# Performance work log

Measured on AMD Instinct MI355X. Metric: run time of the kernel, lower is better.

## Reference

```python
import jax, jax.numpy as jnp
import numpy as np

B, T, D, E, V, EXTRA = 32, 1024, 512, 256, 50257, 200


def setup_inputs() -> dict:
    key = jax.random.key(0)
    ks = jax.random.split(key, 20)
    s = 0.02
    rn = lambda k, shape: jax.random.normal(k, shape, dtype=jnp.float32) * s
    inp = {}
    inp["decoder_input"] = jax.random.randint(ks[0], (B,), 0, V)
    inp["h0"] = rn(ks[1], (B, D))
    inp["c0"] = rn(ks[2], (B, D))
    inp["encoder_outputs"] = rn(ks[3], (B, T, 2 * D))
    inp["encoder_pad_mask"] = jnp.ones((B, T), jnp.float32)
    inp["previous_context_vector"] = rn(ks[4], (B, 2 * D))
    inp["coverage"] = jax.random.uniform(ks[5], (B, T), jnp.float32) * 0.01
    inp["extra_zeros"] = jnp.zeros((B, EXTRA), jnp.float32)
    inp["encoder_input_extra_vocabs"] = jax.random.randint(ks[6], (B, T), 0, V + EXTRA)
    inp["step"] = 1
    inp["embedding"] = rn(ks[7], (V, E))
    inp["W_gx"] = rn(ks[8], (2 * D + E, E)); inp["b_gx"] = jnp.zeros((E,), jnp.float32)
    inp["W_ih"] = rn(ks[9], (E, 4 * D)); inp["W_hh"] = rn(ks[10], (D, 4 * D))
    inp["b_ih"] = jnp.zeros((4 * D,), jnp.float32); inp["b_hh"] = jnp.zeros((4 * D,), jnp.float32)
    inp["W_h"] = rn(ks[11], (2 * D, 2 * D))
    inp["W_c"] = rn(ks[12], (2 * D,))
    inp["W_s"] = rn(ks[13], (2 * D, 2 * D)); inp["b_s"] = jnp.zeros((2 * D,), jnp.float32)
    inp["v"] = rn(ks[14], (2 * D,))
    inp["W_pg"] = rn(ks[15], (4 * D + E,)); inp["b_pg"] = jnp.zeros((1,), jnp.float32)
    inp["W_v1"] = rn(ks[16], (3 * D, D)); inp["b_v1"] = jnp.zeros((D,), jnp.float32)
    inp["W_v2"] = rn(ks[17], (D, V)); inp["b_v2"] = jnp.zeros((V,), jnp.float32)
    return inp


def reference(decoder_input, h0, c0, encoder_outputs, encoder_pad_mask,
              previous_context_vector, coverage, extra_zeros,
              encoder_input_extra_vocabs, step,
              embedding, W_gx, b_gx, W_ih, W_hh, b_ih, b_hh,
              W_h, W_c, W_s, b_s, v, W_pg, b_pg, W_v1, b_v1, W_v2, b_v2):
    # Pointer-generator decoder single step (training path / step>0), coverage on.
    softmax_temperature = 1.0
    emb = embedding[decoder_input]                                  # [B,E]
    x = jnp.concatenate([previous_context_vector, emb], -1) @ W_gx + b_gx  # [B,E]
    # LSTM cell, torch gate order (i, f, g, o)
    gates = x @ W_ih + h0 @ W_hh + b_ih + b_hh                      # [B,4D]
    i, f, g, o = jnp.split(gates, 4, axis=-1)
    c1 = jax.nn.sigmoid(f) * c0 + jax.nn.sigmoid(i) * jnp.tanh(g)
    h1 = jax.nn.sigmoid(o) * jnp.tanh(c1)                           # [B,D]
    dec_hat = jnp.concatenate([h1, c1], -1)                         # [B,2D]
    # Bahdanau additive attention with coverage feature
    enc_feat = encoder_outputs @ W_h                                # [B,T,2D]
    dec_feat = dec_hat @ W_s + b_s                                  # [B,2D]
    cov_feat = coverage[..., None] * W_c                            # [B,T,2D]
    energy = jnp.tanh(enc_feat + dec_feat[:, None, :] + cov_feat)
    scores = energy @ v                                             # [B,T]
    att = jax.nn.softmax(scores / softmax_temperature, axis=-1) * encoder_pad_mask
    att = att / att.sum(-1, keepdims=True)                          # renormalized
    context = jnp.einsum('bt,btd->bd', att, encoder_outputs)        # [B,2D]
    coverage_next = coverage + att
    # pointer-generator gate
    pg_in = jnp.concatenate([context, dec_hat, x], -1)              # [B,4D+E]
    p_gen = jax.nn.sigmoid(pg_in @ W_pg + b_pg)[:, None]            # [B,1]
    out = jnp.concatenate([h1, context], -1)                        # [B,3D]
    logits = ((out @ W_v1 + b_v1) @ W_v2 + b_v2) / softmax_temperature
    vocab_dist = jax.nn.softmax(logits, axis=-1)                    # [B,V]
    vd_oov = jnp.concatenate([p_gen * vocab_dist, extra_zeros], 1)  # [B,V+EXTRA]
    att_oov = (1.0 - p_gen) * att                                   # [B,T]
    rows = jnp.arange(B)[:, None]
    vocab_dist_final = vd_oov.at[rows, encoder_input_extra_vocabs].add(att_oov)
    return (vocab_dist_final, (h1, c1), context, att, coverage_next)
```

## Files before the change

kernel.cpp:

```cpp
#include <hip/hip_runtime.h>
#include <hip/hip_bf16.h>

typedef __attribute__((ext_vector_type(4))) float f32x4;
typedef __attribute__((ext_vector_type(8))) short s16x8;
typedef __attribute__((ext_vector_type(4))) short s16x4;

#define DEVINL __device__ __forceinline__

static constexpr int BB = 32, TT = 1024, DD = 512, EE = 256, VV = 50257, EXTRA = 200;
static constexpr int D2 = 1024;
static constexpr int VE = VV + EXTRA;
static constexpr long MM = (long)BB * TT;
static constexpr int VPAD = 50304;

DEVINL unsigned short f2bf(float x) {
    union { float f; unsigned int u; } c; c.f = x;
    unsigned int u = c.u;
    u += 0x7fffu + ((u >> 16) & 1u);
    return (unsigned short)(u >> 16);
}
DEVINL float bf2f(unsigned short h) {
    union { unsigned int u; float f; } c; c.u = ((unsigned int)h) << 16;
    return c.f;
}
DEVINL float sigmoidf_(float x) { return 1.0f / (1.0f + __expf(-x)); }
DEVINL float tanh_fast(float x) {
    x = fminf(15.f, fmaxf(-15.f, x));
    float e = __expf(2.f * x);
    return (e - 1.f) / (e + 1.f);
}
DEVINL void gl16(const void* g, void* l) {
    __builtin_amdgcn_global_load_lds((__attribute__((address_space(1))) void*)g,
                                     (__attribute__((address_space(3))) void*)l, 16, 0, 0);
}

__global__ void k_transpose_wh(const float* __restrict__ Wh, unsigned short* __restrict__ WhT) {
    __shared__ float tile[32][33];
    int n0 = blockIdx.x * 32, k0 = blockIdx.y * 32;
    int tx = threadIdx.x, ty = threadIdx.y;
    #pragma unroll
    for (int i = 0; i < 4; i++)
        tile[ty + i * 8][tx] = Wh[(long)(k0 + ty + i * 8) * D2 + n0 + tx];
    __syncthreads();
    #pragma unroll
    for (int i = 0; i < 4; i++) {
        int n = n0 + ty + i * 8;
        int kcol = (k0 + tx) ^ ((n & 7) << 3);
        WhT[(long)n * D2 + kcol] = f2bf(tile[tx][ty + i * 8]);
    }
}

__global__ void k_enc2bf(const float* __restrict__ enc, unsigned short* __restrict__ dst) {
    long idx = (long)blockIdx.x * 256 + threadIdx.x;
    int m  = (int)(idx >> 7);
    int k2 = (int)(idx & 127) * 8;
    int s  = (m & 7) << 3;
    const float* src = enc + (long)m * 1024 + (k2 ^ s);
    f32x4 a = *(const f32x4*)src;
    f32x4 b = *(const f32x4*)(src + 4);
    s16x8 h;
    h[0] = (short)f2bf(a[0]); h[1] = (short)f2bf(a[1]); h[2] = (short)f2bf(a[2]); h[3] = (short)f2bf(a[3]);
    h[4] = (short)f2bf(b[0]); h[5] = (short)f2bf(b[1]); h[6] = (short)f2bf(b[2]); h[7] = (short)f2bf(b[3]);
    *(s16x8*)(dst + (long)m * 1024 + k2) = h;
}

__global__ void k_wv2t(const float* __restrict__ Wv2, unsigned short* __restrict__ out) {
    __shared__ float tile[32][33];
    int v0 = blockIdx.x * 32, k0 = blockIdx.y * 32;
    int tx = threadIdx.x, ty = threadIdx.y;
    #pragma unroll
    for (int i = 0; i < 4; i++) {
        int k = k0 + ty + i * 8;
        int v = v0 + tx;
        tile[ty + i * 8][tx] = (v < VV) ? Wv2[(long)k * VV + v] : 0.f;
    }
    __syncthreads();
    #pragma unroll
    for (int i = 0; i < 4; i++) {
        int v = v0 + ty + i * 8;
        int kcol = (k0 + tx) ^ ((v & 7) << 3);
        out[(long)v * 512 + kcol] = f2bf(tile[tx][ty + i * 8]);
    }
}

__global__ __launch_bounds__(512) void k_x(
    const int* __restrict__ dec_in, const float* __restrict__ pcv,
    const float* __restrict__ embt, const float* __restrict__ Wgx,
    const float* __restrict__ bgx, float* __restrict__ xbuf) {
    __shared__ float xs[1280];
    __shared__ float sred[8][64];
    int b = blockIdx.x, n0 = blockIdx.y * 64;
    int tid = threadIdx.x, nl = tid & 63, ks = tid >> 6;
    long er = (long)dec_in[b] * EE;
    for (int i = tid; i < 1280; i += 512)
        xs[i] = (i < 1024) ? pcv[b * 1024 + i] : embt[er + i - 1024];
    __syncthreads();
    float acc = 0.f;
    for (int k = ks * 160; k < ks * 160 + 160; ++k)
        acc += xs[k] * Wgx[(long)k * EE + n0 + nl];
    sred[ks][nl] = acc;
    __syncthreads();
    if (tid < 64) {
        int n = n0 + tid;
        float s = bgx[n];
        #pragma unroll
        for (int i = 0; i < 8; i++) s += sred[i][tid];
        xbuf[b * EE + n] = s;
    }
}

__global__ __launch_bounds__(512) void k_lstm(
    const float* __restrict__ xbuf, const float* __restrict__ h0,
    const float* __restrict__ c0, const float* __restrict__ Wih,
    const float* __restrict__ Whh, const float* __restrict__ bih,
    const float* __restrict__ bhh, float* __restrict__ h1o,
    float* __restrict__ c1o, float* __restrict__ dechat) {
    __shared__ float xs[768];
    __shared__ float sred[4][8][64];
    int b = blockIdx.x, d0 = blockIdx.y * 64;
    int tid = threadIdx.x, dl = tid & 63, ks = tid >> 6;
    for (int i = tid; i < 768; i += 512)
        xs[i] = (i < 256) ? xbuf[b * 256 + i] : h0[b * 512 + i - 256];
    __syncthreads();
    float a0 = 0, a1 = 0, a2 = 0, a3 = 0;
    for (int k = ks * 96; k < ks * 96 + 96; ++k) {
        float xv = xs[k];
        const float* wr = (k < 256) ? (Wih + (long)k * 2048) : (Whh + (long)(k - 256) * 2048);
        a0 += xv * wr[d0 + dl];        a1 += xv * wr[512 + d0 + dl];
        a2 += xv * wr[1024 + d0 + dl]; a3 += xv * wr[1536 + d0 + dl];
    }
    sred[0][ks][dl] = a0; sred[1][ks][dl] = a1; sred[2][ks][dl] = a2; sred[3][ks][dl] = a3;
    __syncthreads();
    if (tid < 64) {
        int d = d0 + tid;
        float gi = bih[d] + bhh[d];
        float gf = bih[512 + d] + bhh[512 + d];
        float gg = bih[1024 + d] + bhh[1024 + d];
        float go = bih[1536 + d] + bhh[1536 + d];
        #pragma unroll
        for (int s = 0; s < 8; s++) {
            gi += sred[0][s][tid]; gf += sred[1][s][tid];
            gg += sred[2][s][tid]; go += sred[3][s][tid];
        }
        float c1 = sigmoidf_(gf) * c0[b * 512 + d] + sigmoidf_(gi) * tanh_fast(gg);
        float h1 = sigmoidf_(go) * tanh_fast(c1);
        h1o[b * 512 + d] = h1; c1o[b * 512 + d] = c1;
        dechat[b * 1024 + d] = h1; dechat[b * 1024 + 512 + d] = c1;
    }
}

__global__ __launch_bounds__(512) void k_decfeat(
    const float* __restrict__ dechat, const float* __restrict__ Ws,
    const float* __restrict__ bs, float* __restrict__ decfeat) {
    __shared__ float xs[1024];
    __shared__ float sred[8][64];
    int b = blockIdx.x, n0 = blockIdx.y * 64;
    int tid = threadIdx.x, nl = tid & 63, ks = tid >> 6;
    for (int i = tid; i < 1024; i += 512) xs[i] = dechat[b * 1024 + i];
    __syncthreads();
    float acc = 0.f;
    for (int k = ks * 128; k < ks * 128 + 128; ++k)
        acc += xs[k] * Ws[(long)k * 1024 + n0 + nl];
    sred[ks][nl] = acc;
    __syncthreads();
    if (tid < 64) {
        int n = n0 + tid;
        float s = bs[n];
        #pragma unroll
        for (int i = 0; i < 8; i++) s += sred[i][tid];
        decfeat[b * 1024 + n] = s;
    }
}

__global__ __launch_bounds__(512) void k_scores(
    const unsigned short* __restrict__ encswz, const unsigned short* __restrict__ whtswz,
    const float* __restrict__ decfeat, const float* __restrict__ cov,
    const float* __restrict__ Wc, const float* __restrict__ vvec,
    float* __restrict__ scorep) {
    __shared__ __align__(16) unsigned short As[128 * 64];
    __shared__ __align__(16) unsigned short Bs[256 * 64];
    __shared__ float sred[4][128];
    const int tid = threadIdx.x;
    const int lane = tid & 63, wave = tid >> 6;
    const int wid = __builtin_amdgcn_readfirstlane(wave);
    const int g = lane >> 4, c = lane & 15;
    const int wm = wave >> 2, wn = wave & 3;

    const int bid = blockIdx.x;
    const int xcd = bid & 7, t = bid >> 3;
    const int mt = xcd * 32 + (t >> 2), nt = t & 3;
    const long m0 = (long)mt * 128;
    const int n0 = nt * 256;
    const int bblk = mt >> 3;

    const int arow = wid * 16 + (lane >> 3);
    const int axo  = (lane & 7) * 8;
    const int brow = wid * 32 + (lane >> 3);
    unsigned short* aBase = &As[wid * 1024];
    unsigned short* bBase = &Bs[wid * 2048];

    f32x4 acc[4][4];
    #pragma unroll
    for (int i = 0; i < 4; i++)
        #pragma unroll
        for (int j = 0; j < 4; j++) acc[i][j] = (f32x4){0.f, 0.f, 0.f, 0.f};

    const int sx = (c & 7) << 3;

    for (int kt = 0; kt < 16; ++kt) {
        const int k0 = kt * 64;
        __syncthreads();
        gl16(encswz + (m0 + arow) * 1024 + k0 + axo,       aBase);
        gl16(encswz + (m0 + arow + 8) * 1024 + k0 + axo,   aBase + 512);
        gl16(whtswz + (long)(n0 + brow) * 1024 + k0 + axo,        bBase);
        gl16(whtswz + (long)(n0 + brow + 8) * 1024 + k0 + axo,    bBase + 512);
        gl16(whtswz + (long)(n0 + brow + 16) * 1024 + k0 + axo,   bBase + 1024);
        gl16(whtswz + (long)(n0 + brow + 24) * 1024 + k0 + axo,   bBase + 1536);
        __syncthreads();
        #pragma unroll
        for (int kk = 0; kk < 2; ++kk) {
            const int kse = (kk * 32 + g * 8) ^ sx;
            s16x8 af[4], bfj[4];
            #pragma unroll
            for (int i = 0; i < 4; i++) af[i] = *(const s16x8*)&As[(wm * 64 + i * 16 + c) * 64 + kse];
            #pragma unroll
            for (int j = 0; j < 4; j++) bfj[j] = *(const s16x8*)&Bs[(wn * 64 + j * 16 + c) * 64 + kse];
            #pragma unroll
            for (int i = 0; i < 4; i++)
                #pragma unroll
                for (int j = 0; j < 4; j++)
                    acc[i][j] = __builtin_amdgcn_mfma_f32_16x16x32_bf16(af[i], bfj[j], acc[i][j], 0, 0, 0);
        }
    }
    float dfv[4], wcv[4], vvj[4];
    #pragma unroll
    for (int j = 0; j < 4; j++) {
        int col = n0 + wn * 64 + j * 16 + c;
        dfv[j] = decfeat[bblk * D2 + col];
        wcv[j] = Wc[col];
        vvj[j] = vvec[col];
    }
    float sAcc[4][4];
    #pragma unroll
    for (int i = 0; i < 4; i++) {
        #pragma unroll
        for (int r = 0; r < 4; r++) {
            const long m = m0 + wm * 64 + i * 16 + g * 4 + r;
            const float covm = cov[m];
            float su = 0.f;
            #pragma unroll
            for (int j = 0; j < 4; j++) {
                float e = acc[i][j][r] + dfv[j] + covm * wcv[j];
                su += tanh_fast(e) * vvj[j];
            }
            su += __shfl_xor(su, 1); su += __shfl_xor(su, 2);
            su += __shfl_xor(su, 4); su += __shfl_xor(su, 8);
            sAcc[i][r] = su;
        }
    }
    if (c == 0) {
        #pragma unroll
        for (int i = 0; i < 4; i++)
            #pragma unroll
            for (int r = 0; r < 4; r++)
                sred[wn][wm * 64 + i * 16 + g * 4 + r] = sAcc[i][r];
    }
    __syncthreads();
    if (tid < 128)
        scorep[(long)nt * MM + m0 + tid] = sred[0][tid] + sred[1][tid] + sred[2][tid] + sred[3][tid];
}

__global__ void k_softmax(const float* __restrict__ scorep, const float* __restrict__ mask,
                          const float* __restrict__ cov, float* __restrict__ att,
                          float* __restrict__ covn) {
    int b = blockIdx.x, tid = threadIdx.x;
    __shared__ float sm[8];
    float sv[4];
    float mx = -1e30f;
    #pragma unroll
    for (int i = 0; i < 4; i++) {
        long idx = (long)b * TT + tid + 256 * i;
        sv[i] = scorep[idx] + scorep[MM + idx] + scorep[2 * MM + idx] + scorep[3 * MM + idx];
        mx = fmaxf(mx, sv[i]);
    }
    for (int o = 32; o; o >>= 1) mx = fmaxf(mx, __shfl_xor(mx, o));
    if ((tid & 63) == 0) sm[tid >> 6] = mx;
    __syncthreads();
    mx = fmaxf(fmaxf(sm[0], sm[1]), fmaxf(sm[2], sm[3]));
    __syncthreads();
    float e[4]; float s = 0.f;
    #pragma unroll
    for (int i = 0; i < 4; i++) { e[i] = __expf(sv[i] - mx); s += e[i]; }
    for (int o = 32; o; o >>= 1) s += __shfl_xor(s, o);
    if ((tid & 63) == 0) sm[tid >> 6] = s;
    __syncthreads();
    s = sm[0] + sm[1] + sm[2] + sm[3];
    __syncthreads();
    float inv = 1.f / s;
    float am[4]; float s2 = 0.f;
    #pragma unroll
    for (int i = 0; i < 4; i++) { am[i] = e[i] * inv * mask[b * TT + tid + 256 * i]; s2 += am[i]; }
    for (int o = 32; o; o >>= 1) s2 += __shfl_xor(s2, o);
    if ((tid & 63) == 0) sm[tid >> 6] = s2;
    __syncthreads();
    s2 = sm[0] + sm[1] + sm[2] + sm[3];
    float inv2 = 1.f / s2;
    #pragma unroll
    for (int i = 0; i < 4; i++) {
        int t = tid + 256 * i;
        float a = am[i] * inv2;
        att[b * TT + t] = a;
        covn[b * TT + t] = cov[b * TT + t] + a;
    }
}

__global__ void k_context(const unsigned short* __restrict__ encswz, const float* __restrict__ att,
                          float* __restrict__ part) {
    int b = blockIdx.x, tc = blockIdx.y;
    int d4 = threadIdx.x;
    float a0 = 0, a1 = 0, a2 = 0, a3 = 0;
    const float* ab = att + b * TT;
    for (int t = tc * 64; t < tc * 64 + 64; ++t) {
        float a = ab[t];
        int sx = (t & 7) << 3;
        const unsigned short* ep = encswz + ((long)b * TT + t) * D2 + ((d4 * 4) ^ sx);
        s16x4 ev = *(const s16x4*)ep;
        a0 += a * bf2f((unsigned short)ev[0]); a1 += a * bf2f((unsigned short)ev[1]);
        a2 += a * bf2f((unsigned short)ev[2]); a3 += a * bf2f((unsigned short)ev[3]);
    }
    float* pp = part + (long)tc * BB * D2 + b * D2 + d4 * 4;
    pp[0] = a0; pp[1] = a1; pp[2] = a2; pp[3] = a3;
}

__global__ void k_ctxreduce(const float* __restrict__ part, float* __restrict__ ctx) {
    int i = blockIdx.x * 256 + threadIdx.x;
    float s = 0.f;
    #pragma unroll
    for (int p = 0; p < 16; p++) s += part[(long)p * BB * D2 + i];
    ctx[i] = s;
}

__global__ void k_pgen(const float* __restrict__ ctx, const float* __restrict__ dechat,
                       const float* __restrict__ xbuf, const float* __restrict__ Wpg,
                       const float* __restrict__ bpg, float* __restrict__ pgen) {
    int b = blockIdx.x, tid = threadIdx.x;
    __shared__ float sm[8];
    float acc = 0.f;
    for (int k = tid; k < D2; k += 256)
        acc += ctx[b * D2 + k] * Wpg[k] + dechat[b * D2 + k] * Wpg[D2 + k];
    acc += xbuf[b * EE + tid] * Wpg[2 * D2 + tid];
    for (int o = 32; o; o >>= 1) acc += __shfl_xor(acc, o);
    if ((tid & 63) == 0) sm[tid >> 6] = acc;
    __syncthreads();
    if (tid == 0) {
        float t = sm[0] + sm[1] + sm[2] + sm[3];
        pgen[b] = sigmoidf_(t + bpg[0]);
    }
}

__global__ __launch_bounds__(512) void k_hidden(
    const float* __restrict__ h1, const float* __restrict__ ctx,
    const float* __restrict__ Wv1, const float* __restrict__ bv1,
    unsigned short* __restrict__ hbf) {
    __shared__ float xs[1536];
    __shared__ float sred[8][64];
    int b = blockIdx.x, n0 = blockIdx.y * 64;
    int tid = threadIdx.x, nl = tid & 63, ks = tid >> 6;
    for (int i = tid; i < 1536; i += 512)
        xs[i] = (i < 512) ? h1[b * 512 + i] : ctx[b * 1024 + i - 512];
    __syncthreads();
    float acc = 0.f;
    for (int k = ks * 192; k < ks * 192 + 192; ++k)
        acc += xs[k] * Wv1[(long)k * 512 + n0 + nl];
    sred[ks][nl] = acc;
    __syncthreads();
    if (tid < 64) {
        int n = n0 + tid;
        float s = bv1[n];
        #pragma unroll
        for (int i = 0; i < 8; i++) s += sred[i][tid];
        hbf[b * 512 + n] = f2bf(s);
    }
}

__global__ __launch_bounds__(256) void k_logits(const unsigned short* __restrict__ hbf,
                                                const unsigned short* __restrict__ wv2t,
                                                const float* __restrict__ bv2,
                                                float* __restrict__ logits) {
    __shared__ __align__(16) unsigned short Bs[64 * 128];
    const int tid = threadIdx.x;
    const int lane = tid & 63, wave = tid >> 6;
    const int wid = __builtin_amdgcn_readfirstlane(wave);
    const int g = lane >> 4, c = lane & 15;
    const int wm = wave >> 1, wn = wave & 1;
    const long v0 = (long)blockIdx.x * 64;

    const int srow = wid * 16 + (lane >> 4);
    const int scol = (lane & 15) * 8;
    unsigned short* bBase = &Bs[wid * 16 * 128];

    f32x4 acc[2];
    acc[0] = (f32x4){0.f, 0.f, 0.f, 0.f};
    acc[1] = (f32x4){0.f, 0.f, 0.f, 0.f};
    const int sx = (c & 7) << 3;

    for (int kt = 0; kt < 4; ++kt) {
        const int k0 = kt * 128;
        __syncthreads();
        #pragma unroll
        for (int i = 0; i < 4; i++)
            gl16(wv2t + (v0 + srow + i * 4) * 512 + k0 + scol, bBase + i * 512);
        __syncthreads();
        #pragma unroll
        for (int kk = 0; kk < 4; ++kk) {
            const int kse = (kk * 32 + g * 8) ^ sx;
            s16x8 af = *(const s16x8*)&hbf[(wm * 16 + c) * 512 + k0 + (kk * 32 + g * 8)];
            s16x8 bf0 = *(const s16x8*)&Bs[(wn * 32 + c) * 128 + kse];
            s16x8 bf1 = *(const s16x8*)&Bs[(wn * 32 + 16 + c) * 128 + kse];
            acc[0] = __builtin_amdgcn_mfma_f32_16x16x32_bf16(af, bf0, acc[0], 0, 0, 0);
            acc[1] = __builtin_amdgcn_mfma_f32_16x16x32_bf16(af, bf1, acc[1], 0, 0, 0);
        }
    }
    #pragma unroll
    for (int j = 0; j < 2; j++) {
        long v = v0 + wn * 32 + j * 16 + c;
        if (v < VV) {
            float bvv = bv2[v];
            #pragma unroll
            for (int r = 0; r < 4; r++) {
                int b = wm * 16 + g * 4 + r;
                logits[(long)b * VV + v] = acc[j][r] + bvv;
            }
        }
    }
}

__global__ __launch_bounds__(1024) void k_vocab_all(
    const float* __restrict__ logits, const float* __restrict__ pgen,
    const float* __restrict__ extraz, const float* __restrict__ att,
    const int* __restrict__ eiv, float* __restrict__ out0) {
    int b = blockIdx.x, tid = threadIdx.x;
    __shared__ float sm[16];
    const float* lr = logits + (long)b * VV;
    float mx = -1e30f;
    for (int v = tid; v < VV; v += 1024) mx = fmaxf(mx, lr[v]);
    for (int o = 32; o; o >>= 1) mx = fmaxf(mx, __shfl_xor(mx, o));
    if ((tid & 63) == 0) sm[tid >> 6] = mx;
    __syncthreads();
    #pragma unroll
    for (int i = 0; i < 16; i++) mx = fmaxf(mx, sm[i]);
    __syncthreads();
    float s = 0.f;
    for (int v = tid; v < VV; v += 1024) s += __expf(lr[v] - mx);
    for (int o = 32; o; o >>= 1) s += __shfl_xor(s, o);
    if ((tid & 63) == 0) sm[tid >> 6] = s;
    __syncthreads();
    s = 0.f;
    #pragma unroll
    for (int i = 0; i < 16; i++) s += sm[i];
    float pg = pgen[b];
    float inv = pg / s;
    float* orow = out0 + (long)b * VE;
    for (int v = tid; v < VV; v += 1024) orow[v] = __expf(lr[v] - mx) * inv;
    if (tid < EXTRA) orow[VV + tid] = extraz[b * EXTRA + tid];
    __syncthreads();
    float a = (1.f - pg) * att[b * TT + tid];
    atomicAdd(orow + eiv[b * TT + tid], a);
}

extern "C" void kernel_launch(void* const* d_in, const int* in_sizes, int n_in,
                              void* d_out, int out_size, void* d_ws, size_t ws_size,
                              hipStream_t stream) {
    const int*   dec_in = (const int*)d_in[0];
    const float* h0     = (const float*)d_in[1];
    const float* c0     = (const float*)d_in[2];
    const float* enc    = (const float*)d_in[3];
    const float* mask   = (const float*)d_in[4];
    const float* pcv    = (const float*)d_in[5];
    const float* cov    = (const float*)d_in[6];
    const float* extraz = (const float*)d_in[7];
    const int*   eiv    = (const int*)d_in[8];
    const float* embt   = (const float*)d_in[10];
    const float* Wgx    = (const float*)d_in[11];
    const float* bgx    = (const float*)d_in[12];
    const float* Wih    = (const float*)d_in[13];
    const float* Whh    = (const float*)d_in[14];
    const float* bih    = (const float*)d_in[15];
    const float* bhh    = (const float*)d_in[16];
    const float* Wh     = (const float*)d_in[17];
    const float* Wc     = (const float*)d_in[18];
    const float* Ws     = (const float*)d_in[19];
    const float* bs     = (const float*)d_in[20];
    const float* vv     = (const float*)d_in[21];
    const float* Wpg    = (const float*)d_in[22];
    const float* bpg    = (const float*)d_in[23];
    const float* Wv1    = (const float*)d_in[24];
    const float* bv1    = (const float*)d_in[25];
    const float* Wv2    = (const float*)d_in[26];
    const float* bv2    = (const float*)d_in[27];

    float* out = (float*)d_out;
    float* out_vd  = out;
    float* out_h1  = out + (long)BB * VE;
    float* out_c1  = out_h1 + BB * DD;
    float* out_ctx = out_c1 + BB * DD;
    float* out_att = out_ctx + BB * D2;
    float* out_cov = out_att + BB * TT;

    char* p = (char*)d_ws;
    unsigned short* whtswz = (unsigned short*)p; p += (size_t)D2 * D2 * 2;
    float* xbuf    = (float*)p;  p += (size_t)BB * EE * 4;
    float* dechat  = (float*)p;  p += (size_t)BB * D2 * 4;
    float* decfeat = (float*)p;  p += (size_t)BB * D2 * 4;
    float* scorep  = (float*)p;  p += (size_t)4 * MM * 4;
    float* pgen    = (float*)p;  p += 256;
    unsigned short* hbf = (unsigned short*)p; p += (size_t)BB * DD * 2 + 256;
    float* ctxpart = (float*)p;  p += (size_t)16 * BB * D2 * 4;
    float* logits  = (float*)p;  p += (size_t)BB * VV * 4;
    unsigned short* encswz = (unsigned short*)p; p += (size_t)MM * D2 * 2;
    unsigned short* wv2t   = (unsigned short*)p; p += (size_t)VPAD * DD * 2;

    k_transpose_wh<<<dim3(32, 32), dim3(32, 8), 0, stream>>>(Wh, whtswz);
    k_enc2bf<<<16384, 256, 0, stream>>>(enc, encswz);
    k_x<<<dim3(BB, 4), 512, 0, stream>>>(dec_in, pcv, embt, Wgx, bgx, xbuf);
    k_lstm<<<dim3(BB, 8), 512, 0, stream>>>(xbuf, h0, c0, Wih, Whh, bih, bhh, out_h1, out_c1, dechat);
    k_decfeat<<<dim3(BB, 16), 512, 0, stream>>>(dechat, Ws, bs, decfeat);
    k_scores<<<1024, 512, 0, stream>>>(encswz, whtswz, decfeat, cov, Wc, vv, scorep);
    k_softmax<<<BB, 256, 0, stream>>>(scorep, mask, cov, out_att, out_cov);
    k_context<<<dim3(BB, 16), 256, 0, stream>>>(encswz, out_att, ctxpart);
    k_ctxreduce<<<(BB * D2) / 256, 256, 0, stream>>>(ctxpart, out_ctx);
    k_pgen<<<BB, 256, 0, stream>>>(out_ctx, dechat, xbuf, Wpg, bpg, pgen);
    k_hidden<<<dim3(BB, 8), 512, 0, stream>>>(out_h1, out_ctx, Wv1, bv1, hbf);
    k_wv2t<<<dim3(VPAD / 32, 16), dim3(32, 8), 0, stream>>>(Wv2, wv2t);
    k_logits<<<VPAD / 64, 256, 0, stream>>>(hbf, wv2t, bv2, logits);
    k_vocab_all<<<BB, 1024, 0, stream>>>(logits, pgen, extraz, out_att, eiv, out_vd);
}
```

Measured before the change: 277.9 us.

## Fuse Wv2 transpose and bf16 conversion into the logits MFMA kernel

Removes the separate k_wv2t pass that transposed the fp32 output projection into a swizzled bf16 workspace. k_logits now reads fp32 Wv2 directly and converts each pair of k-rows to packed bf16. It writes them into a padded, swizzled LDS tile, which cuts one full read/write round trip over the large vocab weight. The trade-off is less contiguous global loads (256-byte row segments, unaligned because VV is odd), more conversion ALU inside the GEMM, and a scalar tail path for the last block.

```diff
diff --git a/kernel.cpp b/kernel.cpp
--- a/kernel.cpp
+++ b/kernel.cpp
@@ -62,25 +62,6 @@
     h[0] = (short)f2bf(a[0]); h[1] = (short)f2bf(a[1]); h[2] = (short)f2bf(a[2]); h[3] = (short)f2bf(a[3]);
     h[4] = (short)f2bf(b[0]); h[5] = (short)f2bf(b[1]); h[6] = (short)f2bf(b[2]); h[7] = (short)f2bf(b[3]);
     *(s16x8*)(dst + (long)m * 1024 + k2) = h;
-}
-
-__global__ void k_wv2t(const float* __restrict__ Wv2, unsigned short* __restrict__ out) {
-    __shared__ float tile[32][33];
-    int v0 = blockIdx.x * 32, k0 = blockIdx.y * 32;
-    int tx = threadIdx.x, ty = threadIdx.y;
-    #pragma unroll
-    for (int i = 0; i < 4; i++) {
-        int k = k0 + ty + i * 8;
-        int v = v0 + tx;
-        tile[ty + i * 8][tx] = (v < VV) ? Wv2[(long)k * VV + v] : 0.f;
-    }
-    __syncthreads();
-    #pragma unroll
-    for (int i = 0; i < 4; i++) {
-        int v = v0 + ty + i * 8;
-        int kcol = (k0 + tx) ^ ((v & 7) << 3);
-        out[(long)v * 512 + kcol] = f2bf(tile[tx][ty + i * 8]);
-    }
 }
 
 __global__ __launch_bounds__(512) void k_x(
@@ -384,39 +365,60 @@
 }
 
 __global__ __launch_bounds__(256) void k_logits(const unsigned short* __restrict__ hbf,
-                                                const unsigned short* __restrict__ wv2t,
+                                                const float* __restrict__ Wv2,
                                                 const float* __restrict__ bv2,
                                                 float* __restrict__ logits) {
-    __shared__ __align__(16) unsigned short Bs[64 * 128];
+    constexpr int PITCH = 136;
+    __shared__ __align__(16) unsigned short Bs[64 * PITCH];
     const int tid = threadIdx.x;
     const int lane = tid & 63, wave = tid >> 6;
-    const int wid = __builtin_amdgcn_readfirstlane(wave);
     const int g = lane >> 4, c = lane & 15;
     const int wm = wave >> 1, wn = wave & 1;
     const long v0 = (long)blockIdx.x * 64;
-
-    const int srow = wid * 16 + (lane >> 4);
-    const int scol = (lane & 15) * 8;
-    unsigned short* bBase = &Bs[wid * 16 * 128];
+    const bool tail = (v0 + 64 > VV);
+
+    const int vg = tid & 15, kr = tid >> 4;
 
     f32x4 acc[2];
     acc[0] = (f32x4){0.f, 0.f, 0.f, 0.f};
     acc[1] = (f32x4){0.f, 0.f, 0.f, 0.f};
-    const int sx = (c & 7) << 3;
+    const int sxr = (c & 7) << 3;
 
     for (int kt = 0; kt < 4; ++kt) {
         const int k0 = kt * 128;
         __syncthreads();
         #pragma unroll
-        for (int i = 0; i < 4; i++)
-            gl16(wv2t + (v0 + srow + i * 4) * 512 + k0 + scol, bBase + i * 512);
+        for (int pi = 0; pi < 4; ++pi) {
+            const int ka = k0 + kr * 8 + pi * 2;
+            f32x4 wa, wb;
+            if (!tail) {
+                wa = *(const f32x4*)&Wv2[(long)ka * VV + v0 + vg * 4];
+                wb = *(const f32x4*)&Wv2[(long)(ka + 1) * VV + v0 + vg * 4];
+            } else {
+                #pragma unroll
+                for (int j = 0; j < 4; j++) {
+                    long v = v0 + vg * 4 + j;
+                    long vs = (v < VV) ? v : (VV - 1);
+                    wa[j] = Wv2[(long)ka * VV + vs];
+                    wb[j] = Wv2[(long)(ka + 1) * VV + vs];
+                }
+            }
+            #pragma unroll
+            for (int j = 0; j < 4; j++) {
+                int vl = vg * 4 + j;
+                int ks = (kr * 8 + pi * 2) ^ ((vl & 7) << 3);
+                unsigned int pack = (unsigned int)f2bf(wa[j]) | ((unsigned int)f2bf(wb[j]) << 16);
+                *(unsigned int*)&Bs[vl * PITCH + ks] = pack;
+            }
+        }
         __syncthreads();
         #pragma unroll
         for (int kk = 0; kk < 4; ++kk) {
-            const int kse = (kk * 32 + g * 8) ^ sx;
-            s16x8 af = *(const s16x8*)&hbf[(wm * 16 + c) * 512 + k0 + (kk * 32 + g * 8)];
-            s16x8 bf0 = *(const s16x8*)&Bs[(wn * 32 + c) * 128 + kse];
-            s16x8 bf1 = *(const s16x8*)&Bs[(wn * 32 + 16 + c) * 128 + kse];
+            const int koff = kk * 32 + g * 8;
+            const int kse = koff ^ sxr;
+            s16x8 af = *(const s16x8*)&hbf[(wm * 16 + c) * 512 + k0 + koff];
+            s16x8 bf0 = *(const s16x8*)&Bs[(wn * 32 + c) * PITCH + kse];
+            s16x8 bf1 = *(const s16x8*)&Bs[(wn * 32 + 16 + c) * PITCH + kse];
             acc[0] = __builtin_amdgcn_mfma_f32_16x16x32_bf16(af, bf0, acc[0], 0, 0, 0);
             acc[1] = __builtin_amdgcn_mfma_f32_16x16x32_bf16(af, bf1, acc[1], 0, 0, 0);
         }
@@ -518,7 +520,6 @@
     float* ctxpart = (float*)p;  p += (size_t)16 * BB * D2 * 4;
     float* logits  = (float*)p;  p += (size_t)BB * VV * 4;
     unsigned short* encswz = (unsigned short*)p; p += (size_t)MM * D2 * 2;
-    unsigned short* wv2t   = (unsigned short*)p; p += (size_t)VPAD * DD * 2;
 
     k_transpose_wh<<<dim3(32, 32), dim3(32, 8), 0, stream>>>(Wh, whtswz);
     k_enc2bf<<<16384, 256, 0, stream>>>(enc, encswz);
@@ -531,7 +532,6 @@
     k_ctxreduce<<<(BB * D2) / 256, 256, 0, stream>>>(ctxpart, out_ctx);
     k_pgen<<<BB, 256, 0, stream>>>(out_ctx, dechat, xbuf, Wpg, bpg, pgen);
     k_hidden<<<dim3(BB, 8), 512, 0, stream>>>(out_h1, out_ctx, Wv1, bv1, hbf);
-    k_wv2t<<<dim3(VPAD / 32, 16), dim3(32, 8), 0, stream>>>(Wv2, wv2t);
-    k_logits<<<VPAD / 64, 256, 0, stream>>>(hbf, wv2t, bv2, logits);
+    k_logits<<<VPAD / 64, 256, 0, stream>>>(hbf, Wv2, bv2, logits);
     k_vocab_all<<<BB, 1024, 0, stream>>>(logits, pgen, extraz, out_att, eiv, out_vd);
 }
```

After: 253.2 us. 8.9% less time.
